# Optimization experiments

Hardware: AMD Instinct MI355X
Metric: run time of the kernel (lower is better)

Reference implementation:

```python
import jax, jax.numpy as jnp
import numpy as np

N_NODES = 100000
N_GRAPHS = 256
N_EDGES = 800000


def gcn_conv(x, W, b, src, dst):
    """PyG GCNConv: self-loops + symmetric deg^-1/2 normalization + scatter-add."""
    h = x @ W  # [N, F_out]
    # degree on graph with self-loops (edge weight 1)
    deg = jax.ops.segment_sum(jnp.ones((src.shape[0],), h.dtype), dst,
                              num_segments=N_NODES) + 1.0
    dinv = jax.lax.rsqrt(deg)  # deg^-1/2, deg >= 1 so finite
    norm = dinv[src] * dinv[dst]  # [E]
    msg = h[src] * norm[:, None]  # gather + scale, [E, F_out]
    agg = jax.ops.segment_sum(msg, dst, num_segments=N_NODES)
    # self-loop contribution: dinv[i]^2 * h[i]
    agg = agg + h * (dinv * dinv)[:, None]
    return agg + b


def setup_inputs() -> dict:
    key = jax.random.key(0)
    ks = jax.random.split(key, 16)
    inp = {
        "x": jax.random.normal(ks[0], (N_NODES, 114), jnp.float32),
        "edge_index": jax.random.randint(ks[1], (2, N_EDGES), 0, N_NODES, jnp.int64)
        if jax.config.jax_enable_x64 else jax.random.randint(ks[1], (2, N_EDGES), 0, N_NODES, jnp.int32),
        "batch": jnp.sort(jax.random.randint(ks[2], (N_NODES,), 0, N_GRAPHS,
                                             jnp.int32)),
        "W1": jax.random.normal(ks[3], (114, 230), jnp.float32) * 0.09,
        "b1": jax.random.normal(ks[4], (230,), jnp.float32) * 0.01,
        "W2": jax.random.normal(ks[5], (230, 115), jnp.float32) * 0.07,
        "b2": jax.random.normal(ks[6], (115,), jnp.float32) * 0.01,
        "Wg": jax.random.normal(ks[7], (115, 64), jnp.float32) * 0.09,
        "bg": jax.random.normal(ks[8], (64,), jnp.float32) * 0.01,
        "Wf": jax.random.normal(ks[9], (64, 32), jnp.float32) * 0.12,
        "bf": jax.random.normal(ks[10], (32,), jnp.float32) * 0.01,
        "Wo": jax.random.normal(ks[11], (32, 1), jnp.float32) * 0.17,
        "bo": jax.random.normal(ks[12], (1,), jnp.float32) * 0.01,
    }
    return inp


def reference(x, edge_index, batch, W1, b1, W2, b2, Wg, bg, Wf, bf, Wo, bo):
    src, dst = edge_index[0], edge_index[1]
    h = jax.nn.relu(gcn_conv(x, W1, b1, src, dst))
    # dropout p=0.2 is identity at inference (training=False)
    h = jax.nn.relu(gcn_conv(h, W2, b2, src, dst))
    # global max pool over graphs; h >= 0 after relu so clamp empty segments to 0
    pooled = jax.ops.segment_max(h, batch, num_segments=N_GRAPHS)
    pooled = jnp.maximum(pooled, 0.0)  # [G, 115]
    g = jax.nn.relu(pooled @ Wg + bg)
    g = jax.nn.relu(g @ Wf + bf)
    return g @ Wo + bo  # [G, 1]
```

## Files before the change

### kernel.cpp

```cpp
#include <hip/hip_runtime.h>
#include <hip/hip_bf16.h>
#include <hip/hip_fp16.h>

#define NN 100000
#define NG 256
#define NE 800000

constexpr int F0 = 114;
constexpr int F1 = 230;
constexpr int F2 = 115;
constexpr int MPAD = 100096;

typedef _Float16 __attribute__((ext_vector_type(8))) f16x8;
typedef __attribute__((ext_vector_type(4))) float f32x4;
typedef __attribute__((ext_vector_type(8))) unsigned short u16x8;

__device__ __forceinline__ unsigned short f2h_bits(float x) {
  _Float16 h = (_Float16)x;
  return __builtin_bit_cast(unsigned short, h);
}
__device__ __forceinline__ float h_bits2f(unsigned short u) {
  return (float)__builtin_bit_cast(_Float16, u);
}

__device__ __forceinline__ void bar_nodrain() {
  asm volatile("s_waitcnt lgkmcnt(0)" ::: "memory");
  __builtin_amdgcn_s_barrier();
}


__global__ void k_count(const int* __restrict__ dst, int* __restrict__ cnt) {
  int e = blockIdx.x * blockDim.x + threadIdx.x;
  if (e < NE) atomicAdd(&cnt[dst[e]], 1);
}

constexpr int SCAN_T = 256;
constexpr int SCAN_E = 1024;
constexpr int NB = (NN + SCAN_E - 1) / SCAN_E;

__global__ void k_scan1(const int* __restrict__ cnt, int* __restrict__ off,
                        int* __restrict__ bsum, float* __restrict__ dinv) {
  __shared__ int s[SCAN_T];
  int b = blockIdx.x, t = threadIdx.x;
  int base = b * SCAN_E + t * 4;
  int v0 = 0, v1 = 0, v2 = 0, v3 = 0;
  if (base + 0 < NN) v0 = cnt[base + 0];
  if (base + 1 < NN) v1 = cnt[base + 1];
  if (base + 2 < NN) v2 = cnt[base + 2];
  if (base + 3 < NN) v3 = cnt[base + 3];
  if (base + 0 < NN) dinv[base + 0] = rsqrtf((float)v0 + 1.0f);
  if (base + 1 < NN) dinv[base + 1] = rsqrtf((float)v1 + 1.0f);
  if (base + 2 < NN) dinv[base + 2] = rsqrtf((float)v2 + 1.0f);
  if (base + 3 < NN) dinv[base + 3] = rsqrtf((float)v3 + 1.0f);
  int sum = v0 + v1 + v2 + v3;
  s[t] = sum;
  __syncthreads();
  for (int ofs = 1; ofs < SCAN_T; ofs <<= 1) {
    int x = (t >= ofs) ? s[t - ofs] : 0;
    __syncthreads();
    s[t] += x;
    __syncthreads();
  }
  int excl = s[t] - sum;
  if (base + 0 < NN) off[base + 0] = excl;
  if (base + 1 < NN) off[base + 1] = excl + v0;
  if (base + 2 < NN) off[base + 2] = excl + v0 + v1;
  if (base + 3 < NN) off[base + 3] = excl + v0 + v1 + v2;
  if (t == SCAN_T - 1) bsum[b] = s[t];
}

__global__ void k_scan3(int* __restrict__ off, const int* __restrict__ bsum,
                        int* __restrict__ cur) {
  __shared__ int pre;
  int b = blockIdx.x, t = threadIdx.x;
  int seg = b >> 2;
  if (t < 64) {
    int s = 0;
    for (int j = t; j < seg; j += 64) s += bsum[j];
#pragma unroll
    for (int o = 1; o < 64; o <<= 1) s += __shfl_xor(s, o);
    if (t == 0) pre = s;
  }
  __syncthreads();
  int i = b * 256 + t;
  if (i < NN) {
    int v = off[i] + pre;
    off[i] = v;
    cur[i] = v;
  }
  if (i == NN) off[NN] = NE;
}

__global__ void k_place(const int* __restrict__ src, const int* __restrict__ dst,
                        int* __restrict__ cur, int* __restrict__ srcs) {
  int e = blockIdx.x * blockDim.x + threadIdx.x;
  if (e >= NE) return;
  int p = atomicAdd(&cur[dst[e]], 1);
  srcs[p] = src[e];
}


__global__ void k_prepx(const float* __restrict__ x, const float* __restrict__ dinv,
                        unsigned short* __restrict__ xd) {
  int n = blockIdx.x, f = threadIdx.x;
  float v = (f < F0) ? x[(size_t)n * F0 + f] * dinv[n] : 0.0f;
  xd[(size_t)n * 128 + f] = f2h_bits(v);
}


template <bool POOL>
__global__ __launch_bounds__(256) void k_gatherw(
    const unsigned short* __restrict__ tab, const float* __restrict__ dinv,
    const int* __restrict__ off, const int* __restrict__ srcs,
    const float* __restrict__ b2, const int* __restrict__ batch,
    unsigned short* __restrict__ outh, float* __restrict__ pooled) {
  __shared__ float smax[4][128];
  __shared__ int sg[4];
  int w = threadIdx.x >> 6, lane = threadIdx.x & 63;
  int n = blockIdx.x * 4 + w;
  int grp = lane >> 4, sub = lane & 15;
  int fb = sub * 8;

  float acc[8] = {0.f, 0.f, 0.f, 0.f, 0.f, 0.f, 0.f, 0.f};
  int j0 = off[n], j1 = off[n + 1];
  for (int base = j0; base <= j1; base += 16) {
    int row[4];
    u16x8 v[4];
    bool has[4];
#pragma unroll
    for (int c = 0; c < 4; ++c) {
      int je = base + c * 4 + grp;
      row[c] = (je < j1) ? srcs[je] : ((je == j1) ? n : -1);
      has[c] = row[c] >= 0;
    }
#pragma unroll
    for (int c = 0; c < 4; ++c)
      if (has[c]) v[c] = *(const u16x8*)&tab[(size_t)row[c] * 128 + fb];
#pragma unroll
    for (int c = 0; c < 4; ++c)
      if (has[c]) {
#pragma unroll
        for (int u = 0; u < 8; ++u) acc[u] += h_bits2f(v[c][u]);
      }
  }
#pragma unroll
  for (int u = 0; u < 8; ++u) {
    acc[u] += __shfl_xor(acc[u], 16);
    acc[u] += __shfl_xor(acc[u], 32);
  }
  float dn = dinv[n];

  if constexpr (!POOL) {
    if (grp == 0) {
      u16x8 o;
#pragma unroll
      for (int u = 0; u < 8; ++u) o[u] = f2h_bits(acc[u] * dn);
      *(u16x8*)&outh[(size_t)n * 128 + fb] = o;
    }
  } else {
    if (grp == 0) {
#pragma unroll
      for (int u = 0; u < 8; ++u) {
        int f = fb + u;
        float bb = (f < F2) ? b2[f] : 0.0f;
        smax[w][f] = fmaxf(acc[u] * dn + bb, 0.0f);
      }
      if (sub == 0) sg[w] = batch[n];
    }
    __syncthreads();
    int t = threadIdx.x;
    if (t < 128) {
      int g0 = sg[0];
      bool same = (sg[1] == g0) & (sg[2] == g0) & (sg[3] == g0);
      if (same) {
        float m = fmaxf(fmaxf(smax[0][t], smax[1][t]),
                        fmaxf(smax[2][t], smax[3][t]));
        if (t < F2 && m > 0.0f)
          atomicMax((int*)&pooled[g0 * F2 + t], __float_as_int(m));
      } else {
        for (int ww = 0; ww < 4; ++ww) {
          float m = smax[ww][t];
          if (t < F2 && m > 0.0f)
            atomicMax((int*)&pooled[sg[ww] * F2 + t], __float_as_int(m));
        }
      }
    }
  }
}


__global__ void k_prepB2(const float* __restrict__ W1, const float* __restrict__ W2,
                         unsigned short* __restrict__ B1h, unsigned short* __restrict__ B1l,
                         unsigned short* __restrict__ B2h, unsigned short* __restrict__ B2l) {
  int b = blockIdx.x, t = threadIdx.x;
  if (b < 128) {
    int n = b * 2 + (t >> 7), k = t & 127;
    float v = (k < F0 && n < F1) ? W1[(size_t)k * F1 + n] : 0.0f;
    unsigned short h = f2h_bits(v);
    unsigned short l = f2h_bits(v - h_bits2f(h));
    B1h[(size_t)n * 128 + k] = h;
    B1l[(size_t)n * 128 + k] = l;
  } else {
    int n = b - 128, k = t;
    float v = (k < F1 && n < F2) ? W2[(size_t)k * F2 + n] : 0.0f;
    unsigned short h = f2h_bits(v);
    unsigned short l = f2h_bits(v - h_bits2f(h));
    B2h[(size_t)n * 256 + k] = h;
    B2l[(size_t)n * 256 + k] = l;
  }
}


__global__ __launch_bounds__(256) void k_fused(
    const unsigned short* __restrict__ A,
    const unsigned short* __restrict__ B1h, const unsigned short* __restrict__ B1l,
    const unsigned short* __restrict__ B2h, const unsigned short* __restrict__ B2l,
    const float* __restrict__ b1, const float* __restrict__ dscale,
    unsigned short* __restrict__ td) {
  __shared__ char lds[81920];
  char* h1B = lds;
  char* AsB = lds + 32768;
  char* Bs0 = lds + 49152;
  char* Bs1 = lds + 65536;

  const int t = threadIdx.x;
  const int m0 = blockIdx.x * 64;
  const int lane = t & 63, w = t >> 6;
  const int r = lane & 15;
  const int kq = lane >> 4;
  const int kb16 = kq * 16;
  const int rq = kq * 4;
  const int wc = w * 32;
  const int swr = (r & 7) << 4;
  const int arow = t >> 2, aseg = t & 3, aswz = (arow & 7) << 4;
  const int brow = t >> 1, bseg = t & 1, bswz = (brow & 7) << 4;

  {
    size_t ga = (size_t)(m0 + arow) * 128 + aseg * 32;
#pragma unroll
    for (int v = 0; v < 4; ++v) {
      u16x8 d = *(const u16x8*)&A[ga + v * 8];
      *(u16x8*)(AsB + arow * 256 + ((aseg * 64 + v * 16) ^ aswz)) = d;
    }
  }
  u16x8 ph[4], pl[4];
  {
    size_t gb = (size_t)brow * 128 + bseg * 32;
#pragma unroll
    for (int v = 0; v < 4; ++v) {
      ph[v] = *(const u16x8*)&B1h[gb + v * 8];
      pl[v] = *(const u16x8*)&B1l[gb + v * 8];
    }
  }

  f32x4 acc1[4][2], acc2[4][2];
#pragma unroll
  for (int i = 0; i < 4; ++i)
#pragma unroll
    for (int j = 0; j < 2; ++j) {
      acc1[i][j] = (f32x4){0.f, 0.f, 0.f, 0.f};
      acc2[i][j] = (f32x4){0.f, 0.f, 0.f, 0.f};
    }

#pragma unroll
  for (int rd = 0; rd < 8; ++rd) {
    bar_nodrain();
#pragma unroll
    for (int v = 0; v < 4; ++v) {
      const int bo = (bseg * 64 + v * 16) ^ bswz;
      *(u16x8*)(Bs0 + brow * 128 + bo) = ph[v];
      *(u16x8*)(Bs1 + brow * 128 + bo) = pl[v];
    }
    if (rd < 7) {
      const int nr = rd + 1;
      const unsigned short* Gh = (nr < 4) ? B1h : B2h;
      const unsigned short* Gl = (nr < 4) ? B1l : B2l;
      const size_t gb = (nr < 4)
          ? (size_t)((nr >> 1) * 128 + brow) * 128 + (nr & 1) * 64 + bseg * 32
          : (size_t)brow * 256 + (nr - 4) * 64 + bseg * 32;
#pragma unroll
      for (int v = 0; v < 4; ++v) {
        ph[v] = *(const u16x8*)&Gh[gb + v * 8];
        pl[v] = *(const u16x8*)&Gl[gb + v * 8];
      }
    }
    bar_nodrain();

    if (rd < 4) {
      const int kc = rd & 1;
#pragma unroll
      for (int ks = 0; ks < 2; ++ks) {
        f16x8 av[4], bh[2], bl[2];
#pragma unroll
        for (int i = 0; i < 4; ++i)
          av[i] = *(const f16x8*)(AsB + (i * 16 + r) * 256 +
                                  ((kc * 128 + ks * 64 + kb16) ^ swr));
#pragma unroll
        for (int j = 0; j < 2; ++j) {
          const int row = wc + j * 16 + r;
          const int bo = (ks * 64 + kb16) ^ swr;
          bh[j] = *(const f16x8*)(Bs0 + row * 128 + bo);
          bl[j] = *(const f16x8*)(Bs1 + row * 128 + bo);
        }
#pragma unroll
        for (int i = 0; i < 4; ++i)
#pragma unroll
          for (int j = 0; j < 2; ++j)
            acc1[i][j] = __builtin_amdgcn_mfma_f32_16x16x32_f16(av[i], bl[j], acc1[i][j], 0, 0, 0);
#pragma unroll
        for (int i = 0; i < 4; ++i)
#pragma unroll
          for (int j = 0; j < 2; ++j)
            acc1[i][j] = __builtin_amdgcn_mfma_f32_16x16x32_f16(av[i], bh[j], acc1[i][j], 0, 0, 0);
      }
      if (rd == 1 || rd == 3) {
        const int h = rd >> 1;
#pragma unroll
        for (int i = 0; i < 4; ++i)
#pragma unroll
          for (int j = 0; j < 2; ++j) {
            const int nl = wc + j * 16 + r;
            const int n = h * 128 + nl;
            const bool val = n < F1;
            const float bb = val ? b1[n] : 0.0f;
#pragma unroll
            for (int q = 0; q < 4; ++q) {
              const int ml = i * 16 + rq + q;
              const float v = val ? fmaxf(acc1[i][j][q] + bb, 0.0f) : 0.0f;
              *(unsigned short*)(h1B + ml * 512 + ((n * 2) ^ ((ml & 7) << 4))) = f2h_bits(v);
            }
          }
#pragma unroll
        for (int i = 0; i < 4; ++i)
#pragma unroll
          for (int j = 0; j < 2; ++j) acc1[i][j] = (f32x4){0.f, 0.f, 0.f, 0.f};
      }
    } else {
      const int kc = rd - 4;
#pragma unroll
      for (int ks = 0; ks < 2; ++ks) {
        f16x8 ah[4], bh[2], bl[2];
#pragma unroll
        for (int i = 0; i < 4; ++i) {
          const int row = i * 16 + r;
          ah[i] = *(const f16x8*)(h1B + row * 512 + ((kc * 128 + ks * 64 + kb16) ^ swr));
        }
#pragma unroll
        for (int j = 0; j < 2; ++j) {
          const int row = wc + j * 16 + r;
          const int bo = (ks * 64 + kb16) ^ swr;
          bh[j] = *(const f16x8*)(Bs0 + row * 128 + bo);
          bl[j] = *(const f16x8*)(Bs1 + row * 128 + bo);
        }
#pragma unroll
        for (int i = 0; i < 4; ++i)
#pragma unroll
          for (int j = 0; j < 2; ++j)
            acc2[i][j] = __builtin_amdgcn_mfma_f32_16x16x32_f16(ah[i], bl[j], acc2[i][j], 0, 0, 0);
#pragma unroll
        for (int i = 0; i < 4; ++i)
#pragma unroll
          for (int j = 0; j < 2; ++j)
            acc2[i][j] = __builtin_amdgcn_mfma_f32_16x16x32_f16(ah[i], bh[j], acc2[i][j], 0, 0, 0);
      }
    }
  }

  __syncthreads();
#pragma unroll
  for (int i = 0; i < 4; ++i)
#pragma unroll
    for (int j = 0; j < 2; ++j) {
      const int nl = wc + j * 16 + r;
#pragma unroll
      for (int q = 0; q < 4; ++q) {
        const int ml = i * 16 + rq + q;
        const float v = acc2[i][j][q] * dscale[m0 + ml];
        *(unsigned short*)(h1B + ml * 512 + ((nl * 2) ^ ((ml & 7) << 4))) = f2h_bits(v);
      }
    }
  __syncthreads();
  {
    const int row = t >> 2, seg = t & 3;
    const int swz = (row & 7) << 4;
    const size_t dst = (size_t)(m0 + row) * 128 + seg * 32;
#pragma unroll
    for (int v = 0; v < 4; ++v) {
      u16x8 d = *(const u16x8*)(h1B + row * 512 + ((seg * 64 + v * 16) ^ swz));
      *(u16x8*)&td[dst + v * 8] = d;
    }
  }
}


__global__ void k_mlp(const float* __restrict__ pooled,
                      const float* __restrict__ Wg, const float* __restrict__ bg,
                      const float* __restrict__ Wf, const float* __restrict__ bf,
                      const float* __restrict__ Wo, const float* __restrict__ bo,
                      float* __restrict__ out) {
  __shared__ float sp[F2];
  __shared__ float sg[64];
  __shared__ float sf[32];
  int g = blockIdx.x, t = threadIdx.x;
  for (int f = t; f < F2; f += 64) sp[f] = pooled[g * F2 + f];
  __syncthreads();
  float a = bg[t];
  for (int k = 0; k < F2; ++k) a += sp[k] * Wg[k * 64 + t];
  sg[t] = fmaxf(a, 0.0f);
  __syncthreads();
  if (t < 32) {
    float c = bf[t];
    for (int k = 0; k < 64; ++k) c += sg[k] * Wf[k * 32 + t];
    sf[t] = fmaxf(c, 0.0f);
  }
  __syncthreads();
  if (t == 0) {
    float c = bo[0];
    for (int k = 0; k < 32; ++k) c += sf[k] * Wo[k];
    out[g] = c;
  }
}


extern "C" void kernel_launch(void* const* d_in, const int* in_sizes, int n_in,
                              void* d_out, int out_size, void* d_ws, size_t ws_size,
                              hipStream_t stream) {
  const float* x  = (const float*)d_in[0];
  const int* ei   = (const int*)d_in[1];
  const int* batch = (const int*)d_in[2];
  const float* W1 = (const float*)d_in[3];
  const float* b1 = (const float*)d_in[4];
  const float* W2 = (const float*)d_in[5];
  const float* b2 = (const float*)d_in[6];
  const float* Wg = (const float*)d_in[7];
  const float* bg = (const float*)d_in[8];
  const float* Wf = (const float*)d_in[9];
  const float* bf = (const float*)d_in[10];
  const float* Wo = (const float*)d_in[11];
  const float* bo = (const float*)d_in[12];
  const int* src = ei;
  const int* dst = ei + NE;

  char* p = (char*)d_ws;
  auto alloc4 = [&](size_t units) { void* r = p; p += units * 4; return r; };
  float* dinv  = (float*)alloc4(100224);
  int* cnt     = (int*)alloc4(100224);
  int* off     = (int*)alloc4(100352);
  int* cur     = (int*)alloc4(100224);
  int* bsum    = (int*)alloc4(128);
  int* srcs    = (int*)alloc4(NE);
  unsigned short* xd   = (unsigned short*)alloc4((size_t)NN * 128 / 2);
  unsigned short* aggX = (unsigned short*)alloc4((size_t)MPAD * 128 / 2);
  unsigned short* td   = (unsigned short*)alloc4((size_t)MPAD * 128 / 2);
  unsigned short* Bt1h = (unsigned short*)alloc4(256 * 128 / 2);
  unsigned short* Bt1l = (unsigned short*)alloc4(256 * 128 / 2);
  unsigned short* Bt2h = (unsigned short*)alloc4(128 * 256 / 2);
  unsigned short* Bt2l = (unsigned short*)alloc4(128 * 256 / 2);
  float* pooled = (float*)alloc4((size_t)NG * F2);

  hipMemsetAsync(cnt, 0, 100224 * sizeof(int), stream);
  hipMemsetAsync(pooled, 0, (size_t)NG * F2 * sizeof(float), stream);

  k_count<<<(NE + 255) / 256, 256, 0, stream>>>(dst, cnt);
  k_scan1<<<NB, SCAN_T, 0, stream>>>(cnt, off, bsum, dinv);
  k_scan3<<<(NN + 256) / 256, 256, 0, stream>>>(off, bsum, cur);
  k_place<<<(NE + 255) / 256, 256, 0, stream>>>(src, dst, cur, srcs);

  k_prepB2<<<256, 256, 0, stream>>>(W1, W2, Bt1h, Bt1l, Bt2h, Bt2l);

  k_prepx<<<NN, 128, 0, stream>>>(x, dinv, xd);
  k_gatherw<false><<<NN / 4, 256, 0, stream>>>(xd, dinv, off, srcs,
                                               nullptr, nullptr, aggX, nullptr);

  k_fused<<<MPAD / 64, 256, 0, stream>>>(aggX, Bt1h, Bt1l, Bt2h, Bt2l,
                                         b1, dinv, td);

  k_gatherw<true><<<NN / 4, 256, 0, stream>>>(td, dinv, off, srcs,
                                              b2, batch, nullptr, pooled);

  k_mlp<<<NG, 64, 0, stream>>>(pooled, Wg, bg, Wf, bf, Wo, bo, (float*)d_out);
}
```

Before: 296.3 us.

## Merge place, prepx, weight prep and pool zeroing into one launch; add MFMA priority

Combines the edge placement, x scaling/conversion, weight split-precision prep and pooled-buffer zeroing into a single multi-role kernel dispatched by block index. This cuts three kernel launches and one memset, and the x prep now uses 256-thread blocks. It also wraps the MFMA bursts in the fused GEMM kernel with s_setprio to raise wave priority during matrix math. The merged kernel is branch-divergent by block range, and the independent roles now share one dispatch.

```diff
diff --git a/kernel.cpp b/kernel.cpp
--- a/kernel.cpp
+++ b/kernel.cpp
@@ -91,20 +91,56 @@
   if (i == NN) off[NN] = NE;
 }
 
-__global__ void k_place(const int* __restrict__ src, const int* __restrict__ dst,
-                        int* __restrict__ cur, int* __restrict__ srcs) {
-  int e = blockIdx.x * blockDim.x + threadIdx.x;
-  if (e >= NE) return;
-  int p = atomicAdd(&cur[dst[e]], 1);
-  srcs[p] = src[e];
-}
-
-
-__global__ void k_prepx(const float* __restrict__ x, const float* __restrict__ dinv,
-                        unsigned short* __restrict__ xd) {
-  int n = blockIdx.x, f = threadIdx.x;
-  float v = (f < F0) ? x[(size_t)n * F0 + f] * dinv[n] : 0.0f;
-  xd[(size_t)n * 128 + f] = f2h_bits(v);
+
+constexpr int FB_PLACE = (NE + 255) / 256;
+constexpr int FB_PREPX = NN / 2;
+constexpr int FB_PREPB = 256;
+constexpr int FB_POOL  = (NG * F2 + 255) / 256;
+
+__global__ __launch_bounds__(256) void k_fatB(
+    const int* __restrict__ src, const int* __restrict__ dst,
+    int* __restrict__ cur, int* __restrict__ srcs,
+    const float* __restrict__ x, const float* __restrict__ dinv,
+    unsigned short* __restrict__ xd,
+    const float* __restrict__ W1, const float* __restrict__ W2,
+    unsigned short* __restrict__ B1h, unsigned short* __restrict__ B1l,
+    unsigned short* __restrict__ B2h, unsigned short* __restrict__ B2l,
+    float* __restrict__ pooled) {
+  int b = blockIdx.x, t = threadIdx.x;
+  if (b < FB_PLACE) {
+    int e = b * 256 + t;
+    if (e < NE) {
+      int p = atomicAdd(&cur[dst[e]], 1);
+      srcs[p] = src[e];
+    }
+  } else if (b < FB_PLACE + FB_PREPX) {
+    int bb = b - FB_PLACE;
+    int n = bb * 2 + (t >> 7);
+    int f = t & 127;
+    float v = (f < F0) ? x[(size_t)n * F0 + f] * dinv[n] : 0.0f;
+    xd[(size_t)n * 128 + f] = f2h_bits(v);
+  } else if (b < FB_PLACE + FB_PREPX + FB_PREPB) {
+    int bb = b - (FB_PLACE + FB_PREPX);
+    if (bb < 128) {
+      int n = bb * 2 + (t >> 7), k = t & 127;
+      float v = (k < F0 && n < F1) ? W1[(size_t)k * F1 + n] : 0.0f;
+      unsigned short h = f2h_bits(v);
+      unsigned short l = f2h_bits(v - h_bits2f(h));
+      B1h[(size_t)n * 128 + k] = h;
+      B1l[(size_t)n * 128 + k] = l;
+    } else {
+      int n = bb - 128, k = t;
+      float v = (k < F1 && n < F2) ? W2[(size_t)k * F2 + n] : 0.0f;
+      unsigned short h = f2h_bits(v);
+      unsigned short l = f2h_bits(v - h_bits2f(h));
+      B2h[(size_t)n * 256 + k] = h;
+      B2l[(size_t)n * 256 + k] = l;
+    }
+  } else {
+    int bb = b - (FB_PLACE + FB_PREPX + FB_PREPB);
+    int i = bb * 256 + t;
+    if (i < NG * F2) pooled[i] = 0.0f;
+  }
 }
 
 
@@ -189,28 +225,6 @@
 }
 
 
-__global__ void k_prepB2(const float* __restrict__ W1, const float* __restrict__ W2,
-                         unsigned short* __restrict__ B1h, unsigned short* __restrict__ B1l,
-                         unsigned short* __restrict__ B2h, unsigned short* __restrict__ B2l) {
-  int b = blockIdx.x, t = threadIdx.x;
-  if (b < 128) {
-    int n = b * 2 + (t >> 7), k = t & 127;
-    float v = (k < F0 && n < F1) ? W1[(size_t)k * F1 + n] : 0.0f;
-    unsigned short h = f2h_bits(v);
-    unsigned short l = f2h_bits(v - h_bits2f(h));
-    B1h[(size_t)n * 128 + k] = h;
-    B1l[(size_t)n * 128 + k] = l;
-  } else {
-    int n = b - 128, k = t;
-    float v = (k < F1 && n < F2) ? W2[(size_t)k * F2 + n] : 0.0f;
-    unsigned short h = f2h_bits(v);
-    unsigned short l = f2h_bits(v - h_bits2f(h));
-    B2h[(size_t)n * 256 + k] = h;
-    B2l[(size_t)n * 256 + k] = l;
-  }
-}
-
-
 __global__ __launch_bounds__(256) void k_fused(
     const unsigned short* __restrict__ A,
     const unsigned short* __restrict__ B1h, const unsigned short* __restrict__ B1l,
@@ -302,6 +316,7 @@
           bh[j] = *(const f16x8*)(Bs0 + row * 128 + bo);
           bl[j] = *(const f16x8*)(Bs1 + row * 128 + bo);
         }
+        __builtin_amdgcn_s_setprio(1);
 #pragma unroll
         for (int i = 0; i < 4; ++i)
 #pragma unroll
@@ -312,6 +327,7 @@
 #pragma unroll
           for (int j = 0; j < 2; ++j)
             acc1[i][j] = __builtin_amdgcn_mfma_f32_16x16x32_f16(av[i], bh[j], acc1[i][j], 0, 0, 0);
+        __builtin_amdgcn_s_setprio(0);
       }
       if (rd == 1 || rd == 3) {
         const int h = rd >> 1;
@@ -352,6 +368,7 @@
           bh[j] = *(const f16x8*)(Bs0 + row * 128 + bo);
           bl[j] = *(const f16x8*)(Bs1 + row * 128 + bo);
         }
+        __builtin_amdgcn_s_setprio(1);
 #pragma unroll
         for (int i = 0; i < 4; ++i)
 #pragma unroll
@@ -362,6 +379,7 @@
 #pragma unroll
           for (int j = 0; j < 2; ++j)
             acc2[i][j] = __builtin_amdgcn_mfma_f32_16x16x32_f16(ah[i], bh[j], acc2[i][j], 0, 0, 0);
+        __builtin_amdgcn_s_setprio(0);
       }
     }
   }
@@ -459,16 +477,15 @@
   float* pooled = (float*)alloc4((size_t)NG * F2);
 
   hipMemsetAsync(cnt, 0, 100224 * sizeof(int), stream);
-  hipMemsetAsync(pooled, 0, (size_t)NG * F2 * sizeof(float), stream);
 
   k_count<<<(NE + 255) / 256, 256, 0, stream>>>(dst, cnt);
   k_scan1<<<NB, SCAN_T, 0, stream>>>(cnt, off, bsum, dinv);
   k_scan3<<<(NN + 256) / 256, 256, 0, stream>>>(off, bsum, cur);
-  k_place<<<(NE + 255) / 256, 256, 0, stream>>>(src, dst, cur, srcs);
-
-  k_prepB2<<<256, 256, 0, stream>>>(W1, W2, Bt1h, Bt1l, Bt2h, Bt2l);
-
-  k_prepx<<<NN, 128, 0, stream>>>(x, dinv, xd);
+
+  k_fatB<<<FB_PLACE + FB_PREPX + FB_PREPB + FB_POOL, 256, 0, stream>>>(
+      src, dst, cur, srcs, x, dinv, xd, W1, W2,
+      Bt1h, Bt1l, Bt2h, Bt2l, pooled);
+
   k_gatherw<false><<<NN / 4, 256, 0, stream>>>(xd, dinv, off, srcs,
                                                nullptr, nullptr, aggX, nullptr);
 
```

New measurement: 291.8 us. About the same (-1.5%).
